# Performance work log

Hardware: AMD Instinct MI355X
Metric: run time of the kernel (lower is better)

The kernel has to match this reference:

```python
import jax, jax.numpy as jnp
import numpy as np

B, E, S, H = 8, 1024, 2048, 16  # batch, embed_dim, seq_len, n_heads
D = E // H                       # per-head hidden dim


def setup_inputs() -> dict:
    key = jax.random.key(0)
    k1, k2 = jax.random.split(key)
    x = jax.random.normal(k1, (B, E, S), dtype=jnp.float32)
    weight = jax.random.normal(k2, (H, S), dtype=jnp.float32)  # nn.Parameter(torch.randn)
    bias = jnp.zeros((H, S), dtype=jnp.float32)                # nn.Parameter(torch.zeros)
    return {"x": x, "weight": weight, "bias": bias}


def _vector_to_matrix(v):
    # v: (H, S) -> M: (H, S, S), M[h, i, j] = v[h, j - i] if j >= i else 0
    h, m = v.shape
    i = jnp.arange(m)[:, None]
    j = jnp.arange(m)[None, :]
    off = j - i  # negative offsets wrap (same as torch fancy indexing) but are masked out
    return jnp.where(j >= i, v[:, off], jnp.zeros((), dtype=v.dtype))


def reference(x, weight, bias):
    b, e, s = x.shape
    h = weight.shape[0]
    d = e // h
    M = _vector_to_matrix(weight)  # (H, S, S)
    # Original: x.view(B,H,D,S).reshape(B*H,D,S) paired with W.repeat_interleave(B,0),
    # i.e. flat index k uses M[k // B]. Group the flat B*H axis into H contiguous
    # blocks of size B so each block shares one Toeplitz matrix (no (B*H,S,S) blowup).
    xg = x.reshape(b * h, d, s).reshape(h, b, d, s)  # block m = M[m]
    out = jnp.einsum('mbds,mst->mbdt', xg, M) + bias[:, None, None, :]
    return out.reshape(b, e, s)
```

## Files before the change

kernel.cpp:

```cpp
#include <hip/hip_runtime.h>
#include <hip/hip_bf16.h>

#define SEQ    2048
#define NHEAD  16
#define RPH    512
#define BM     128
#define BK     64
#define NTH    256

#define WSTRIDE 2184
#define ABUF_E  8192
#define WCOP_E  (2 * ABUF_E)
#define TOT_E   (WCOP_E + 8 * WSTRIDE)

typedef float  f32x4  __attribute__((ext_vector_type(4)));
typedef __bf16 bf16x8 __attribute__((ext_vector_type(8)));

struct PF { float4 v0, v1, v2, v3, v4, v5, v6, v7; };

__device__ __forceinline__ unsigned f2bf(float f) {
    union { __hip_bfloat16 h; unsigned short u; } cv;
    cv.h = __float2bfloat16(f);
    return (unsigned)cv.u;
}

__device__ __forceinline__ uint4 pack8u(float4 a, float4 b) {
    union { bf16x8 v; uint4 u; } r;
    r.v[0] = (__bf16)a.x; r.v[1] = (__bf16)a.y;
    r.v[2] = (__bf16)a.z; r.v[3] = (__bf16)a.w;
    r.v[4] = (__bf16)b.x; r.v[5] = (__bf16)b.y;
    r.v[6] = (__bf16)b.z; r.v[7] = (__bf16)b.w;
    return r.u;
}

#define MFMA16(a, b, c) __builtin_amdgcn_mfma_f32_16x16x32_bf16((a), (b), (c), 0, 0, 0)

#define LOADPF(P, CH)                                                         \
  { const float* g_ = Xp + (size_t)(CH) * BK;                                 \
    P.v0 = *(const float4*)g_;                                                \
    P.v1 = *(const float4*)(g_ + 4);                                          \
    P.v2 = *(const float4*)(g_ + 8 * SEQ);                                    \
    P.v3 = *(const float4*)(g_ + 8 * SEQ + 4);                                \
    P.v4 = *(const float4*)(g_ + 16 * SEQ);                                   \
    P.v5 = *(const float4*)(g_ + 16 * SEQ + 4);                               \
    P.v6 = *(const float4*)(g_ + 24 * SEQ);                                   \
    P.v7 = *(const float4*)(g_ + 24 * SEQ + 4); }

#define WRITEA(AB, P)                                                         \
  { *(uint4*)((AB) + wb0) = pack8u(P.v0, P.v1);                               \
    *(uint4*)((AB) + wb1) = pack8u(P.v2, P.v3);                               \
    *(uint4*)((AB) + wb2) = pack8u(P.v4, P.v5);                               \
    *(uint4*)((AB) + wb3) = pack8u(P.v6, P.v7); }

#define KSTEP(ABC, KS, BASE)                                                  \
  { const int kb_ = (64 * (KS) + kq16) ^ swz;                                 \
    bf16x8 af0 = *(const bf16x8*)((ABC) + Arow0 + kb_);                       \
    bf16x8 af1 = *(const bf16x8*)((ABC) + Arow1 + kb_);                       \
    acc[0][0] = MFMA16(af0, bw[(BASE)    ], acc[0][0]);                       \
    acc[1][0] = MFMA16(af1, bw[(BASE)    ], acc[1][0]);                       \
    acc[0][1] = MFMA16(af0, bw[(BASE) - 1], acc[0][1]);                       \
    acc[1][1] = MFMA16(af1, bw[(BASE) - 1], acc[1][1]);                       \
    acc[0][2] = MFMA16(af0, bw[(BASE) - 2], acc[0][2]);                       \
    acc[1][2] = MFMA16(af1, bw[(BASE) - 2], acc[1][2]);                       \
    acc[0][3] = MFMA16(af0, bw[(BASE) - 3], acc[0][3]);                       \
    acc[1][3] = MFMA16(af1, bw[(BASE) - 3], acc[1][3]);                       \
    acc[0][4] = MFMA16(af0, bw[(BASE) - 4], acc[0][4]);                       \
    acc[1][4] = MFMA16(af1, bw[(BASE) - 4], acc[1][4]);                       \
    acc[0][5] = MFMA16(af0, bw[(BASE) - 5], acc[0][5]);                       \
    acc[1][5] = MFMA16(af1, bw[(BASE) - 5], acc[1][5]);                       \
    acc[0][6] = MFMA16(af0, bw[(BASE) - 6], acc[0][6]);                       \
    acc[1][6] = MFMA16(af1, bw[(BASE) - 6], acc[1][6]);                       \
    acc[0][7] = MFMA16(af0, bw[(BASE) - 7], acc[0][7]);                       \
    acc[1][7] = MFMA16(af1, bw[(BASE) - 7], acc[1][7]); }

__global__ __launch_bounds__(NTH, 2) void mixer_kernel(
    const float* __restrict__ x, const float* __restrict__ wgt,
    const float* __restrict__ bias, float* __restrict__ out)
{
    __shared__ unsigned short smem[TOT_E] __attribute__((aligned(16)));
    char* ab0 = (char*)smem;
    char* ab1 = (char*)smem + ABUF_E * 2;
    unsigned short* wc = smem + WCOP_E;

    const int tid  = threadIdx.x;
    const int lane = tid & 63;
    const int wv   = tid >> 6;

    const int bid  = blockIdx.x;
    const int m    = (bid & 7) + 8 * ((bid >> 3) & 1);
    const int rt   = (bid >> 4) & 3;
    const int pr   = bid >> 6;
    const int ct_hi = 15 - pr;
    const int ct_lo = pr;

    const float* Xb = x   + (size_t)(m * RPH + rt * BM) * SEQ;
    float*       Ob = out + (size_t)(m * RPH + rt * BM) * SEQ;
    const float* wr = wgt  + m * SEQ;
    const float* br = bias + m * SEQ;

    const int sr    = lane >> 3;
    const int sc    = (lane & 7) * 8;
    const int wsw   = ((lane & 7) * 16) ^ (sr << 4);
    const int rbw   = 32 * wv;
    const int wb0   = (rbw + sr)      * 128 + wsw;
    const int wb1   = (rbw + sr + 8)  * 128 + wsw;
    const int wb2   = (rbw + sr + 16) * 128 + wsw;
    const int wb3   = (rbw + sr + 24) * 128 + wsw;
    const float* Xp = Xb + (size_t)(rbw + sr) * SEQ + sc;

    PF pfA, pfB;
    LOADPF(pfA, 0);
    LOADPF(pfB, 1);

    {
        const int t8 = tid * 8;
        const float* g = wr + (2040 - t8);
        float4 lo = *(const float4*)g;
        float4 hi = *(const float4*)(g + 4);
        uint4 v;
        v.x = f2bf(hi.w) | (f2bf(hi.z) << 16);
        v.y = f2bf(hi.y) | (f2bf(hi.x) << 16);
        v.z = f2bf(lo.w) | (f2bf(lo.z) << 16);
        v.w = f2bf(lo.y) | (f2bf(lo.x) << 16);
        *(uint4*)(smem + 8 + t8) = v;
        if (tid < 21) {
            uint4 z = {0u, 0u, 0u, 0u};
            unsigned short* dst = (tid == 0) ? smem
                                 : smem + 8 + 2048 + (tid - 1) * 8;
            *(uint4*)dst = z;
        }
    }
    __syncthreads();

    #pragma unroll
    for (int c = 0; c < 8; ++c) {
        for (int grp = tid; grp < WSTRIDE / 8; grp += NTH) {
            const int i = grp * 8;
            uint4 g0 = *(const uint4*)(smem + 8 + i - 8);
            uint4 g1 = *(const uint4*)(smem + 8 + i);
            unsigned d[9] = {g0.x, g0.y, g0.z, g0.w,
                             g1.x, g1.y, g1.z, g1.w, 0u};
            const int qd = (16 - 2 * c) >> 2;
            uint4 o;
            if (c & 1) {
                o.x = (d[qd]     >> 16) | (d[qd + 1] << 16);
                o.y = (d[qd + 1] >> 16) | (d[qd + 2] << 16);
                o.z = (d[qd + 2] >> 16) | (d[qd + 3] << 16);
                o.w = (d[qd + 3] >> 16) | (d[qd + 4] << 16);
            } else {
                o.x = d[qd];     o.y = d[qd + 1];
                o.z = d[qd + 2]; o.w = d[qd + 3];
            }
            *(uint4*)(wc + c * WSTRIDE + i) = o;
        }
    }
    __syncthreads();

    const int col_low = lane & 15;
    const int kq      = lane >> 4;
    const int kq16    = kq * 16;
    const int swz     = (col_low & 7) << 4;
    const int cpy     = (col_low + 1) & 7;
    const int BcBase  = cpy * WSTRIDE + cpy + 2047 - col_low + 8 * kq;
    const int Arow0   = (rbw      + col_low) * 128;
    const int Arow1   = (rbw + 16 + col_low) * 128;

    #pragma unroll
    for (int half = 0; half < 2; ++half) {
        const int ct  = half ? ct_lo : ct_hi;
        const int t0  = ct << 7;
        const int nch = 2 * (ct + 1);
        const int Bc0 = BcBase - t0;

        if (half) { LOADPF(pfA, 0); LOADPF(pfB, 1); }
        WRITEA(ab0, pfA);

        f32x4 acc[2][8] = {};
        for (int ch = 0; ch < nch; ch += 2) {
            bf16x8 bw[14];
            const unsigned short* bpp = wc + (Bc0 + 64 * ch - 112);
            #pragma unroll
            for (int i = 0; i < 14; ++i)
                bw[i] = *(const bf16x8*)(bpp + 16 * i);

            if (ch + 2 < nch) LOADPF(pfA, ch + 2);
            WRITEA(ab1, pfB);
            __builtin_amdgcn_s_setprio(1);
            KSTEP(ab0, 0, 7);
            KSTEP(ab0, 1, 9);
            __builtin_amdgcn_s_setprio(0);

            if (ch + 3 < nch) LOADPF(pfB, ch + 3);
            if (ch + 2 < nch) WRITEA(ab0, pfA);
            __builtin_amdgcn_s_setprio(1);
            KSTEP(ab1, 0, 11);
            KSTEP(ab1, 1, 13);
            __builtin_amdgcn_s_setprio(0);
        }

        #pragma unroll
        for (int c = 0; c < 8; ++c) {
            const int colg = t0 + 16 * c + col_low;
            const float bv = br[colg];
            #pragma unroll
            for (int a = 0; a < 2; ++a) {
                const int rowl = rbw + 16 * a + 4 * kq;
                #pragma unroll
                for (int r = 0; r < 4; ++r)
                    Ob[(size_t)(rowl + r) * SEQ + colg] = acc[a][c][r] + bv;
            }
        }
    }
}

extern "C" void kernel_launch(void* const* d_in, const int* in_sizes, int n_in,
                              void* d_out, int out_size, void* d_ws, size_t ws_size,
                              hipStream_t stream) {
    const float* x  = (const float*)d_in[0];
    const float* w  = (const float*)d_in[1];
    const float* bs = (const float*)d_in[2];
    float* out = (float*)d_out;
    dim3 grid(512);
    dim3 block(NTH);
    hipLaunchKernelGGL(mixer_kernel, grid, block, 0, stream, x, w, bs, out);
}
```

Before: 46.09 us.

## Load A fragments directly from global into MFMA registers, drop LDS staging

Each lane now loads its own x elements straight from global memory in the MFMA operand layout and converts them to bf16 in registers, instead of writing converted tiles to swizzled LDS buffers and reading them back. This removes the LDS write/read traffic and shrinks shared memory to just the weight copies. In exchange the global loads become less coalesced (each lane reads 32-byte pieces from different rows), which may raise memory transaction cost.

```diff
diff --git a/kernel.cpp b/kernel.cpp
--- a/kernel.cpp
+++ b/kernel.cpp
@@ -9,8 +9,7 @@
 #define NTH    256
 
 #define WSTRIDE 2184
-#define ABUF_E  8192
-#define WCOP_E  (2 * ABUF_E)
+#define WCOP_E  2216
 #define TOT_E   (WCOP_E + 8 * WSTRIDE)
 
 typedef float  f32x4  __attribute__((ext_vector_type(4)));
@@ -24,62 +23,50 @@
     return (unsigned)cv.u;
 }
 
-__device__ __forceinline__ uint4 pack8u(float4 a, float4 b) {
-    union { bf16x8 v; uint4 u; } r;
-    r.v[0] = (__bf16)a.x; r.v[1] = (__bf16)a.y;
-    r.v[2] = (__bf16)a.z; r.v[3] = (__bf16)a.w;
-    r.v[4] = (__bf16)b.x; r.v[5] = (__bf16)b.y;
-    r.v[6] = (__bf16)b.z; r.v[7] = (__bf16)b.w;
-    return r.u;
+__device__ __forceinline__ bf16x8 pack8(float4 a, float4 b) {
+    bf16x8 r;
+    r[0] = (__bf16)a.x; r[1] = (__bf16)a.y; r[2] = (__bf16)a.z; r[3] = (__bf16)a.w;
+    r[4] = (__bf16)b.x; r[5] = (__bf16)b.y; r[6] = (__bf16)b.z; r[7] = (__bf16)b.w;
+    return r;
 }
 
 #define MFMA16(a, b, c) __builtin_amdgcn_mfma_f32_16x16x32_bf16((a), (b), (c), 0, 0, 0)
 
-#define LOADPF(P, CH)                                                         \
-  { const float* g_ = Xp + (size_t)(CH) * BK;                                 \
-    P.v0 = *(const float4*)g_;                                                \
-    P.v1 = *(const float4*)(g_ + 4);                                          \
-    P.v2 = *(const float4*)(g_ + 8 * SEQ);                                    \
-    P.v3 = *(const float4*)(g_ + 8 * SEQ + 4);                                \
-    P.v4 = *(const float4*)(g_ + 16 * SEQ);                                   \
-    P.v5 = *(const float4*)(g_ + 16 * SEQ + 4);                               \
-    P.v6 = *(const float4*)(g_ + 24 * SEQ);                                   \
-    P.v7 = *(const float4*)(g_ + 24 * SEQ + 4); }
-
-#define WRITEA(AB, P)                                                         \
-  { *(uint4*)((AB) + wb0) = pack8u(P.v0, P.v1);                               \
-    *(uint4*)((AB) + wb1) = pack8u(P.v2, P.v3);                               \
-    *(uint4*)((AB) + wb2) = pack8u(P.v4, P.v5);                               \
-    *(uint4*)((AB) + wb3) = pack8u(P.v6, P.v7); }
-
-#define KSTEP(ABC, KS, BASE)                                                  \
-  { const int kb_ = (64 * (KS) + kq16) ^ swz;                                 \
-    bf16x8 af0 = *(const bf16x8*)((ABC) + Arow0 + kb_);                       \
-    bf16x8 af1 = *(const bf16x8*)((ABC) + Arow1 + kb_);                       \
-    acc[0][0] = MFMA16(af0, bw[(BASE)    ], acc[0][0]);                       \
-    acc[1][0] = MFMA16(af1, bw[(BASE)    ], acc[1][0]);                       \
-    acc[0][1] = MFMA16(af0, bw[(BASE) - 1], acc[0][1]);                       \
-    acc[1][1] = MFMA16(af1, bw[(BASE) - 1], acc[1][1]);                       \
-    acc[0][2] = MFMA16(af0, bw[(BASE) - 2], acc[0][2]);                       \
-    acc[1][2] = MFMA16(af1, bw[(BASE) - 2], acc[1][2]);                       \
-    acc[0][3] = MFMA16(af0, bw[(BASE) - 3], acc[0][3]);                       \
-    acc[1][3] = MFMA16(af1, bw[(BASE) - 3], acc[1][3]);                       \
-    acc[0][4] = MFMA16(af0, bw[(BASE) - 4], acc[0][4]);                       \
-    acc[1][4] = MFMA16(af1, bw[(BASE) - 4], acc[1][4]);                       \
-    acc[0][5] = MFMA16(af0, bw[(BASE) - 5], acc[0][5]);                       \
-    acc[1][5] = MFMA16(af1, bw[(BASE) - 5], acc[1][5]);                       \
-    acc[0][6] = MFMA16(af0, bw[(BASE) - 6], acc[0][6]);                       \
-    acc[1][6] = MFMA16(af1, bw[(BASE) - 6], acc[1][6]);                       \
-    acc[0][7] = MFMA16(af0, bw[(BASE) - 7], acc[0][7]);                       \
-    acc[1][7] = MFMA16(af1, bw[(BASE) - 7], acc[1][7]); }
+#define LOADA(P, CH)                                                          \
+  { const float* gA_ = Ar0 + (size_t)(CH) * BK;                               \
+    P.v0 = *(const float4*)gA_;                                               \
+    P.v1 = *(const float4*)(gA_ + 4);                                         \
+    P.v2 = *(const float4*)(gA_ + 32);                                        \
+    P.v3 = *(const float4*)(gA_ + 36);                                        \
+    const float* gB_ = Ar1 + (size_t)(CH) * BK;                               \
+    P.v4 = *(const float4*)gB_;                                               \
+    P.v5 = *(const float4*)(gB_ + 4);                                         \
+    P.v6 = *(const float4*)(gB_ + 32);                                        \
+    P.v7 = *(const float4*)(gB_ + 36); }
+
+#define KSTEP2(AF0, AF1, BASE)                                                \
+  { acc[0][0] = MFMA16(AF0, bw[(BASE)    ], acc[0][0]);                       \
+    acc[1][0] = MFMA16(AF1, bw[(BASE)    ], acc[1][0]);                       \
+    acc[0][1] = MFMA16(AF0, bw[(BASE) - 1], acc[0][1]);                       \
+    acc[1][1] = MFMA16(AF1, bw[(BASE) - 1], acc[1][1]);                       \
+    acc[0][2] = MFMA16(AF0, bw[(BASE) - 2], acc[0][2]);                       \
+    acc[1][2] = MFMA16(AF1, bw[(BASE) - 2], acc[1][2]);                       \
+    acc[0][3] = MFMA16(AF0, bw[(BASE) - 3], acc[0][3]);                       \
+    acc[1][3] = MFMA16(AF1, bw[(BASE) - 3], acc[1][3]);                       \
+    acc[0][4] = MFMA16(AF0, bw[(BASE) - 4], acc[0][4]);                       \
+    acc[1][4] = MFMA16(AF1, bw[(BASE) - 4], acc[1][4]);                       \
+    acc[0][5] = MFMA16(AF0, bw[(BASE) - 5], acc[0][5]);                       \
+    acc[1][5] = MFMA16(AF1, bw[(BASE) - 5], acc[1][5]);                       \
+    acc[0][6] = MFMA16(AF0, bw[(BASE) - 6], acc[0][6]);                       \
+    acc[1][6] = MFMA16(AF1, bw[(BASE) - 6], acc[1][6]);                       \
+    acc[0][7] = MFMA16(AF0, bw[(BASE) - 7], acc[0][7]);                       \
+    acc[1][7] = MFMA16(AF1, bw[(BASE) - 7], acc[1][7]); }
 
 __global__ __launch_bounds__(NTH, 2) void mixer_kernel(
     const float* __restrict__ x, const float* __restrict__ wgt,
     const float* __restrict__ bias, float* __restrict__ out)
 {
     __shared__ unsigned short smem[TOT_E] __attribute__((aligned(16)));
-    char* ab0 = (char*)smem;
-    char* ab1 = (char*)smem + ABUF_E * 2;
     unsigned short* wc = smem + WCOP_E;
 
     const int tid  = threadIdx.x;
@@ -98,19 +85,18 @@
     const float* wr = wgt  + m * SEQ;
     const float* br = bias + m * SEQ;
 
-    const int sr    = lane >> 3;
-    const int sc    = (lane & 7) * 8;
-    const int wsw   = ((lane & 7) * 16) ^ (sr << 4);
-    const int rbw   = 32 * wv;
-    const int wb0   = (rbw + sr)      * 128 + wsw;
-    const int wb1   = (rbw + sr + 8)  * 128 + wsw;
-    const int wb2   = (rbw + sr + 16) * 128 + wsw;
-    const int wb3   = (rbw + sr + 24) * 128 + wsw;
-    const float* Xp = Xb + (size_t)(rbw + sr) * SEQ + sc;
+    const int col_low = lane & 15;
+    const int kq      = lane >> 4;
+    const int rbw     = 32 * wv;
+    const int cpy     = (col_low + 1) & 7;
+    const int BcBase  = cpy * WSTRIDE + cpy + 2047 - col_low + 8 * kq;
+
+    const float* Ar0 = Xb + (size_t)(rbw + col_low) * SEQ + 8 * kq;
+    const float* Ar1 = Ar0 + 16 * (size_t)SEQ;
 
     PF pfA, pfB;
-    LOADPF(pfA, 0);
-    LOADPF(pfB, 1);
+    LOADA(pfA, 0);
+    LOADA(pfB, 1);
 
     {
         const int t8 = tid * 8;
@@ -156,15 +142,6 @@
     }
     __syncthreads();
 
-    const int col_low = lane & 15;
-    const int kq      = lane >> 4;
-    const int kq16    = kq * 16;
-    const int swz     = (col_low & 7) << 4;
-    const int cpy     = (col_low + 1) & 7;
-    const int BcBase  = cpy * WSTRIDE + cpy + 2047 - col_low + 8 * kq;
-    const int Arow0   = (rbw      + col_low) * 128;
-    const int Arow1   = (rbw + 16 + col_low) * 128;
-
     #pragma unroll
     for (int half = 0; half < 2; ++half) {
         const int ct  = half ? ct_lo : ct_hi;
@@ -172,8 +149,7 @@
         const int nch = 2 * (ct + 1);
         const int Bc0 = BcBase - t0;
 
-        if (half) { LOADPF(pfA, 0); LOADPF(pfB, 1); }
-        WRITEA(ab0, pfA);
+        if (half) { LOADA(pfA, 0); LOADA(pfB, 1); }
 
         f32x4 acc[2][8] = {};
         for (int ch = 0; ch < nch; ch += 2) {
@@ -183,18 +159,24 @@
             for (int i = 0; i < 14; ++i)
                 bw[i] = *(const bf16x8*)(bpp + 16 * i);
 
-            if (ch + 2 < nch) LOADPF(pfA, ch + 2);
-            WRITEA(ab1, pfB);
+            bf16x8 a00 = pack8(pfA.v0, pfA.v1);
+            bf16x8 a01 = pack8(pfA.v2, pfA.v3);
+            bf16x8 a10 = pack8(pfA.v4, pfA.v5);
+            bf16x8 a11 = pack8(pfA.v6, pfA.v7);
+            if (ch + 2 < nch) LOADA(pfA, ch + 2);
             __builtin_amdgcn_s_setprio(1);
-            KSTEP(ab0, 0, 7);
-            KSTEP(ab0, 1, 9);
+            KSTEP2(a00, a10, 7);
+            KSTEP2(a01, a11, 9);
             __builtin_amdgcn_s_setprio(0);
 
-            if (ch + 3 < nch) LOADPF(pfB, ch + 3);
-            if (ch + 2 < nch) WRITEA(ab0, pfA);
+            bf16x8 b00 = pack8(pfB.v0, pfB.v1);
+            bf16x8 b01 = pack8(pfB.v2, pfB.v3);
+            bf16x8 b10 = pack8(pfB.v4, pfB.v5);
+            bf16x8 b11 = pack8(pfB.v6, pfB.v7);
+            if (ch + 3 < nch) LOADA(pfB, ch + 3);
             __builtin_amdgcn_s_setprio(1);
-            KSTEP(ab1, 0, 11);
-            KSTEP(ab1, 1, 13);
+            KSTEP2(b00, b10, 11);
+            KSTEP2(b01, b11, 13);
             __builtin_amdgcn_s_setprio(0);
         }
 
```

Result: slower. 72.35 us (+57.0%).
